# Optimization experiments

Measured on AMD Instinct MI355X. Metric: run time of the kernel, lower is better.

The kernel has to match this reference:

```python
import jax, jax.numpy as jnp
import numpy as np

Z = Y = X = 128
H = W = 256
FEAT_CH = 128
PE_DIM = 9
EMB = 128
B, V, NPTS = 2, 4, 65536


def make_grid_zyx():
    zs = jnp.linspace(-1.0, 1.0, Z)
    ys = jnp.linspace(-1.0, 1.0, Y)
    xs = jnp.linspace(-1.0, 1.0, X)
    gz, gy, gx = jnp.meshgrid(zs, ys, xs, indexing='ij')
    return jnp.stack([gz, gy, gx], axis=-1).reshape(-1, 3)  # (Z*Y*X, 3)


def fourier_pe(c):
    # coords + sin/cos at base frequency -> 3+3+3 = 9 dims
    return jnp.concatenate([c, jnp.sin(jnp.pi * c), jnp.cos(jnp.pi * c)], axis=-1)


def bilinear_sample(fm, py, px):
    # fm: (C,H,W); py,px: (n,) pixel coords (align_corners, border clamp) -> (n,C)
    px = jnp.clip(px, 0.0, W - 1.0)
    py = jnp.clip(py, 0.0, H - 1.0)
    x0 = jnp.clip(jnp.floor(px).astype(jnp.int32), 0, W - 2)
    y0 = jnp.clip(jnp.floor(py).astype(jnp.int32), 0, H - 2)
    x1, y1 = x0 + 1, y0 + 1
    wx = px - x0
    wy = py - y0
    f00 = fm[:, y0, x0]; f01 = fm[:, y0, x1]
    f10 = fm[:, y1, x0]; f11 = fm[:, y1, x1]
    top = f00 * (1.0 - wx) + f01 * wx
    bot = f10 * (1.0 - wx) + f11 * wx
    return (top * (1.0 - wy) + bot * wy).T


def inr_mlp(x, w_in, b_in, w1, b1, w2, b2, w_out, b_out):
    # pre-act residual MLP: num_blocks is small & static, loop is fine
    h = jax.nn.relu(x @ w_in + b_in)
    for i in range(w1.shape[0]):
        h = jax.nn.relu(h + jax.nn.relu(h @ w1[i] + b1[i]) @ w2[i] + b2[i])
    return h @ w_out + b_out


def setup_inputs() -> dict:
    key = jax.random.key(0)
    ks = jax.random.split(key, 24)
    s = 0.05
    n = lambda k, shp: jax.random.normal(k, shp, jnp.float32) * s
    return {
        'views': jax.random.normal(ks[0], (B, V, 1, H, W), jnp.float32),
        'angles': jax.random.uniform(ks[1], (B, V), jnp.float32, 0.0, 2.0 * np.pi),
        'idx': jax.random.randint(ks[2], (NPTS,), 0, Z * Y * X, jnp.int32),
        'conv_w': n(ks[3], (FEAT_CH, 1, 3, 3)),
        'conv_b': n(ks[4], (FEAT_CH,)),
        'vw_in': n(ks[5], (FEAT_CH + PE_DIM, 128)), 'vb_in': n(ks[6], (128,)),
        'vw1': n(ks[7], (3, 128, 128)), 'vb1': n(ks[8], (3, 128)),
        'vw2': n(ks[9], (3, 128, 128)), 'vb2': n(ks[10], (3, 128)),
        'vw_out': n(ks[11], (128, EMB)), 'vb_out': n(ks[12], (EMB,)),
        'gw_in': n(ks[13], (EMB, 128)), 'gb_in': n(ks[14], (128,)),
        'gw1': n(ks[15], (2, 128, 128)), 'gb1': n(ks[16], (2, 128)),
        'gw2': n(ks[17], (2, 128, 128)), 'gb2': n(ks[18], (2, 128)),
        'gw_out': n(ks[19], (128, 1)), 'gb_out': n(ks[20], (1,)),
    }


def reference(views, angles, idx, conv_w, conv_b, vw_in, vb_in, vw1, vb1, vw2, vb2,
              vw_out, vb_out, gw_in, gb_in, gw1, gb1, gw2, gb2, gw_out, gb_out):
    Bn, Vn = views.shape[0], views.shape[1]
    npts = idx.shape[0]
    # backbone (U-Net stand-in): 3x3 conv 1->feat_ch + ReLU
    x2d = views.reshape(Bn * Vn, 1, H, W)
    feats = jax.lax.conv_general_dilated(x2d, conv_w, (1, 1), 'SAME',
                                         dimension_numbers=('NCHW', 'OIHW', 'NCHW'))
    feats = jax.nn.relu(feats + conv_b[None, :, None, None]).reshape(Bn, Vn, FEAT_CH, H, W)
    # gather coords for requested voxels, positional encoding
    coords = make_grid_zyx()[idx]                      # (n,3) zyx in [-1,1]
    pe = fourier_pe(coords)                            # (n,9)
    z, y, x = coords[:, 0], coords[:, 1], coords[:, 2]
    ct = jnp.cos(angles)[..., None]                    # (B,V,1)
    st = jnp.sin(angles)[..., None]
    u = x[None, None, :] * ct - y[None, None, :] * st  # rotated in-plane coord (B,V,n)
    v = jnp.broadcast_to(z[None, None, :], u.shape)    # detector vertical = z
    px = (u + 1.0) * 0.5 * (W - 1)
    py = (v + 1.0) * 0.5 * (H - 1)
    f = jax.vmap(jax.vmap(bilinear_sample))(feats, py, px)        # (B,V,n,C)
    pe_b = jnp.broadcast_to(pe[None, None], (Bn, Vn, npts, PE_DIM))
    xin = jnp.concatenate([f, pe_b], axis=-1).reshape(Bn * Vn * npts, FEAT_CH + PE_DIM)
    r = inr_mlp(xin, vw_in, vb_in, vw1, vb1, vw2, vb2, vw_out, vb_out)
    r_mean = r.reshape(Bn, Vn, npts, EMB).mean(axis=1)            # sum over views / V
    yout = inr_mlp(r_mean.reshape(Bn * npts, EMB), gw_in, gb_in, gw1, gb1, gw2, gb2, gw_out, gb_out)
    return yout.reshape(Bn, npts)
```

## Files before the change

kernel.cpp:

```cpp
#include <hip/hip_runtime.h>
#include <math.h>

#define BB 2
#define VV 4
#define NPTSC 65536
#define HH 256
#define WW 256
#define CCH 128
#define PTS 32
#define ROWS (VV * PTS)

typedef __attribute__((ext_vector_type(8))) unsigned short ushort8;
typedef __attribute__((ext_vector_type(4))) unsigned short u16x4;
typedef __attribute__((ext_vector_type(8))) __bf16 bf16x8;
typedef __attribute__((ext_vector_type(4))) float floatx4;

__device__ unsigned short g_feats[(size_t)BB * VV * HH * WW * CCH];

__device__ __forceinline__ float b2f(unsigned short u) {
  unsigned int x = ((unsigned int)u) << 16;
  return __builtin_bit_cast(float, x);
}
__device__ __forceinline__ unsigned short f2b(float f) {
  return __builtin_bit_cast(unsigned short, (__bf16)f);
}

__global__ __launch_bounds__(256) void mvct_pc(
    const float* __restrict__ views, const float* __restrict__ conv_w,
    const float* __restrict__ conv_b,
    const float* __restrict__ vw_in, const float* __restrict__ vw1,
    const float* __restrict__ vw2, const float* __restrict__ vw_out,
    const float* __restrict__ gw_in, const float* __restrict__ gw1,
    const float* __restrict__ gw2, unsigned short* __restrict__ wbuf)
{
  if (blockIdx.x < 2048) {
    __shared__ float rows[2][3][132];
    const int h = threadIdx.x >> 7;
    const int c = threadIdx.x & 127;
    const int bv = blockIdx.x >> 8;
    const int y = blockIdx.x & 255;
    const int xb = h * 128;

    float w[9];
#pragma unroll
    for (int j = 0; j < 9; ++j) w[j] = conv_w[c * 9 + j];
    const float bias = conv_b[c];

    const float* img = views + (size_t)bv * HH * WW;
#pragma unroll
    for (int r = 0; r < 3; ++r) {
      int yy = y - 1 + r;
      for (int xcol = c; xcol < 130; xcol += 128) {
        int xx = xb - 1 + xcol;
        float v = 0.f;
        if (yy >= 0 && yy < HH && xx >= 0 && xx < WW) v = img[yy * WW + xx];
        rows[h][r][xcol] = v;
      }
    }
    __syncthreads();

    unsigned short* orow =
        g_feats + ((size_t)((bv * HH + y) * WW + xb)) * CCH + c;
    float a0 = rows[h][0][0], a1 = rows[h][1][0], a2 = rows[h][2][0];
    float b0 = rows[h][0][1], b1 = rows[h][1][1], b2 = rows[h][2][1];
#pragma unroll 8
    for (int x = 0; x < 128; ++x) {
      float c0 = rows[h][0][x + 2];
      float c1 = rows[h][1][x + 2];
      float c2 = rows[h][2][x + 2];
      float acc = bias
        + a0 * w[0] + b0 * w[1] + c0 * w[2]
        + a1 * w[3] + b1 * w[4] + c1 * w[5]
        + a2 * w[6] + b2 * w[7] + c2 * w[8];
      acc = fmaxf(acc, 0.f);
      orow[(size_t)x * CCH] = f2b(acc);
      a0 = b0; a1 = b1; a2 = b2;
      b0 = c0; b1 = c1; b2 = c2;
    }
  } else {
    int tid = (blockIdx.x - 2048) * 256 + threadIdx.x;
    if (tid >= 217088) return;
    float val;
    if (tid < 20480) {
      int n = tid / 160, k = tid - n * 160;
      val = (k < 137) ? vw_in[k * 128 + n] : 0.f;
    } else {
      int t = tid - 20480;
      const float* src;
      if (t < 49152) { src = vw1; }
      else if (t < 98304) { t -= 49152; src = vw2; }
      else if (t < 114688) { t -= 98304; src = vw_out; }
      else if (t < 131072) { t -= 114688; src = gw_in; }
      else if (t < 163840) { t -= 131072; src = gw1; }
      else { t -= 163840; src = gw2; }
      int i = t >> 14; int r = t & 16383; int n = r >> 7; int k = r & 127;
      val = src[i * 16384 + k * 128 + n];
    }
    wbuf[tid] = f2b(val);
  }
}

struct WReg {
  ushort8 a[2][4];
  floatx4 bs[2];
};

__device__ __forceinline__ WReg wload(const unsigned short* __restrict__ Wt,
                                      const float* __restrict__ bias,
                                      int lane, int ftBase) {
  WReg w;
  const int col = lane & 15, quad = lane >> 4;
#pragma unroll
  for (int ftl = 0; ftl < 2; ++ftl) {
    const int ft = ftBase + ftl;
#pragma unroll
    for (int kk = 0; kk < 4; ++kk)
      w.a[ftl][kk] = *(const ushort8*)(Wt + (ft * 16 + col) * 128 + kk * 32 + quad * 8);
    w.bs[ftl] = *(const floatx4*)(bias + ft * 16 + quad * 4);
  }
  return w;
}

template<int MODE, int NPT>
__device__ __forceinline__ void mlp_c(
    const unsigned short* Act, int lda, const WReg& w,
    const unsigned short* Res, int ldr,
    unsigned short* Dst, int ldd,
    float* racc, int lane, int ftBase)
{
  const int col = lane & 15, quad = lane >> 4;
  auto body = [&](int ptt) {
    ushort8 bfr[4];
#pragma unroll
    for (int kk = 0; kk < 4; ++kk)
      bfr[kk] = *(const ushort8*)(Act + (ptt * 16 + col) * lda + kk * 32 + quad * 8);
#pragma unroll
    for (int ftl = 0; ftl < 2; ++ftl) {
      const int ft = ftBase + ftl;
      floatx4 acc = {0.f, 0.f, 0.f, 0.f};
#pragma unroll
      for (int kk = 0; kk < 4; ++kk)
        acc = __builtin_amdgcn_mfma_f32_16x16x32_bf16(
            __builtin_bit_cast(bf16x8, w.a[ftl][kk]),
            __builtin_bit_cast(bf16x8, bfr[kk]), acc, 0, 0, 0);
      const int row = ptt * 16 + col;
      if constexpr (MODE == 2) {
#pragma unroll
        for (int r = 0; r < 4; ++r)
          racc[(ptt & 1) * 8 + ftl * 4 + r] += acc[r] + w.bs[ftl][r];
      } else {
        u16x4 rv;
        if constexpr (MODE == 1)
          rv = *(const u16x4*)(Res + row * ldr + ft * 16 + quad * 4);
        u16x4 o;
#pragma unroll
        for (int r = 0; r < 4; ++r) {
          float v = acc[r] + w.bs[ftl][r];
          if constexpr (MODE == 1) v += b2f(rv[r]);
          v = fmaxf(v, 0.f);
          o[r] = f2b(v);
        }
        *(u16x4*)(Dst + row * ldd + ft * 16 + quad * 4) = o;
      }
    }
  };
  if constexpr (MODE == 2) {
#pragma unroll
    for (int ptt = 0; ptt < NPT; ++ptt) body(ptt);
  } else {
#pragma unroll 2
    for (int ptt = 0; ptt < NPT; ++ptt) body(ptt);
  }
  __syncthreads();
}

__device__ __forceinline__ void mlp_first(
    const unsigned short* Act, int lda,
    const unsigned short* __restrict__ Wt, const float* __restrict__ bias,
    unsigned short* Dst, int ldd, int lane, int ftBase)
{
  const int col = lane & 15, quad = lane >> 4;
  ushort8 afr[2][5];
  floatx4 bs4[2];
#pragma unroll
  for (int ftl = 0; ftl < 2; ++ftl) {
    const int ft = ftBase + ftl;
#pragma unroll
    for (int kk = 0; kk < 5; ++kk)
      afr[ftl][kk] = *(const ushort8*)(Wt + (ft * 16 + col) * 160 + kk * 32 + quad * 8);
    bs4[ftl] = *(const floatx4*)(bias + ft * 16 + quad * 4);
  }
#pragma unroll 2
  for (int ptt = 0; ptt < (ROWS / 16); ++ptt) {
    ushort8 bfr[5];
#pragma unroll
    for (int kk = 0; kk < 5; ++kk)
      bfr[kk] = *(const ushort8*)(Act + (ptt * 16 + col) * lda + kk * 32 + quad * 8);
#pragma unroll
    for (int ftl = 0; ftl < 2; ++ftl) {
      const int ft = ftBase + ftl;
      floatx4 acc = {0.f, 0.f, 0.f, 0.f};
#pragma unroll
      for (int kk = 0; kk < 5; ++kk)
        acc = __builtin_amdgcn_mfma_f32_16x16x32_bf16(
            __builtin_bit_cast(bf16x8, afr[ftl][kk]),
            __builtin_bit_cast(bf16x8, bfr[kk]), acc, 0, 0, 0);
      const int row = ptt * 16 + col;
      u16x4 o;
#pragma unroll
      for (int r = 0; r < 4; ++r)
        o[r] = f2b(fmaxf(acc[r] + bs4[ftl][r], 0.f));
      *(u16x4*)(Dst + row * ldd + ft * 16 + quad * 4) = o;
    }
  }
  __syncthreads();
}

__global__ __launch_bounds__(256, 2) void mvct_main(
    const float* __restrict__ angles, const int* __restrict__ idx,
    const unsigned short* __restrict__ wbuf,
    const float* __restrict__ vb_in, const float* __restrict__ vb1,
    const float* __restrict__ vb2, const float* __restrict__ vb_out,
    const float* __restrict__ gb_in, const float* __restrict__ gb1,
    const float* __restrict__ gb2, const float* __restrict__ gw_out,
    const float* __restrict__ gb_out,
    float* __restrict__ out)
{
  __shared__ __align__(16) unsigned short X[ROWS][168];
  __shared__ __align__(16) unsigned short Hb[ROWS][136];
  const int tid = threadIdx.x;
  const int lane = tid & 63;
  const int ftBase = (tid >> 6) * 2;
  const int b = blockIdx.x >> 11;
  const int pts0 = (blockIdx.x & 2047) * PTS;

  const unsigned short* w_in_t   = wbuf;
  const unsigned short* vw1_t    = wbuf + 20480;
  const unsigned short* vw2_t    = wbuf + 69632;
  const unsigned short* vw_out_t = wbuf + 118784;
  const unsigned short* gw_in_t  = wbuf + 135168;
  const unsigned short* gw1_t    = wbuf + 151552;
  const unsigned short* gw2_t    = wbuf + 184320;

  const float inv = 2.0f / 127.0f;
  const int col = lane & 15, quad = lane >> 4;

  if (tid < ROWS) {
    int p = tid & (PTS - 1);
    int id = idx[pts0 + p];
    int iz = (id >> 14) & 127, iy = (id >> 7) & 127, ix = id & 127;
    float x = ix * inv - 1.f, y = iy * inv - 1.f, z = iz * inv - 1.f;
    const float PI = 3.14159265358979323846f;
    float pe[9] = {z, y, x, sinf(PI * z), sinf(PI * y), sinf(PI * x),
                   cosf(PI * z), cosf(PI * y), cosf(PI * x)};
#pragma unroll
    for (int j = 0; j < 9; ++j) X[tid][128 + j] = f2b(pe[j]);
    for (int j = 137; j < 160; ++j) X[tid][j] = 0;
  }

#pragma unroll
  for (int v = 0; v < VV; ++v) {
    const int bv = b * VV + v;
    const float ang = angles[bv];
    const float ct = cosf(ang), st = sinf(ang);
    const int cg = tid & 15;
#pragma unroll
    for (int ph = 0; ph < 2; ++ph) {
      const int p = ((tid >> 4) & 15) + ph * 16;
      int id = idx[pts0 + p];
      int iz = (id >> 14) & 127, iy = (id >> 7) & 127, ix = id & 127;
      float x = ix * inv - 1.f, y = iy * inv - 1.f, z = iz * inv - 1.f;
      float u = x * ct - y * st;
      float px = (u + 1.f) * 127.5f, py = (z + 1.f) * 127.5f;
      px = fminf(fmaxf(px, 0.f), 255.f);
      py = fminf(fmaxf(py, 0.f), 255.f);
      int x0 = min((int)px, 254), y0 = min((int)py, 254);
      float wx = px - (float)x0, wy = py - (float)y0;
      const unsigned short* bp =
          g_feats + ((size_t)((bv * HH + y0) * WW + x0)) * CCH + cg * 8;
      ushort8 q00 = *(const ushort8*)bp;
      ushort8 q01 = *(const ushort8*)(bp + CCH);
      ushort8 q10 = *(const ushort8*)(bp + WW * CCH);
      ushort8 q11 = *(const ushort8*)(bp + WW * CCH + CCH);
      float w00 = (1.f - wx) * (1.f - wy), w01 = wx * (1.f - wy);
      float w10 = (1.f - wx) * wy, w11 = wx * wy;
      ushort8 o;
#pragma unroll
      for (int j = 0; j < 8; ++j) {
        float f = w00 * b2f(q00[j]) + w01 * b2f(q01[j]) +
                  w10 * b2f(q10[j]) + w11 * b2f(q11[j]);
        o[j] = f2b(f);
      }
      *(ushort8*)&X[v * PTS + p][cg * 8] = o;
    }
  }
  __syncthreads();

  float racc[16];
#pragma unroll
  for (int i = 0; i < 16; ++i) racc[i] = 0.f;

  WReg wA = wload(vw1_t, vb1, lane, ftBase);
  mlp_first(&X[0][0], 168, w_in_t, vb_in, &Hb[0][0], 136, lane, ftBase);
  WReg wB = wload(vw2_t, vb2, lane, ftBase);
  mlp_c<0, 8>(&Hb[0][0], 136, wA, nullptr, 0, &X[0][0], 168, nullptr,
              lane, ftBase);
  wA = wload(vw1_t + 16384, vb1 + 128, lane, ftBase);
  mlp_c<1, 8>(&X[0][0], 168, wB, &Hb[0][0], 136, &Hb[0][0], 136, nullptr,
              lane, ftBase);
  wB = wload(vw2_t + 16384, vb2 + 128, lane, ftBase);
  mlp_c<0, 8>(&Hb[0][0], 136, wA, nullptr, 0, &X[0][0], 168, nullptr,
              lane, ftBase);
  wA = wload(vw1_t + 32768, vb1 + 256, lane, ftBase);
  mlp_c<1, 8>(&X[0][0], 168, wB, &Hb[0][0], 136, &Hb[0][0], 136, nullptr,
              lane, ftBase);
  wB = wload(vw2_t + 32768, vb2 + 256, lane, ftBase);
  mlp_c<0, 8>(&Hb[0][0], 136, wA, nullptr, 0, &X[0][0], 168, nullptr,
              lane, ftBase);
  wA = wload(vw_out_t, vb_out, lane, ftBase);
  mlp_c<1, 8>(&X[0][0], 168, wB, &Hb[0][0], 136, &Hb[0][0], 136, nullptr,
              lane, ftBase);
  wB = wload(gw_in_t, gb_in, lane, ftBase);
  mlp_c<2, 8>(&Hb[0][0], 136, wA, nullptr, 0, nullptr, 0, racc,
              lane, ftBase);

#pragma unroll
  for (int ph = 0; ph < 2; ++ph)
#pragma unroll
    for (int ftl = 0; ftl < 2; ++ftl) {
      u16x4 o;
#pragma unroll
      for (int r = 0; r < 4; ++r)
        o[r] = f2b(racc[ph * 8 + ftl * 4 + r] * 0.25f);
      *(u16x4*)(&X[ph * 16 + col][(ftBase + ftl) * 16 + quad * 4]) = o;
    }
  __syncthreads();

  wA = wload(gw1_t, gb1, lane, ftBase);
  mlp_c<0, 2>(&X[0][0], 168, wB, nullptr, 0, &Hb[0][0], 136, nullptr,
              lane, ftBase);
  wB = wload(gw2_t, gb2, lane, ftBase);
  mlp_c<0, 2>(&Hb[0][0], 136, wA, nullptr, 0, &X[0][0], 168, nullptr,
              lane, ftBase);
  wA = wload(gw1_t + 16384, gb1 + 128, lane, ftBase);
  mlp_c<1, 2>(&X[0][0], 168, wB, &Hb[0][0], 136, &Hb[0][0], 136, nullptr,
              lane, ftBase);
  wB = wload(gw2_t + 16384, gb2 + 128, lane, ftBase);
  mlp_c<0, 2>(&Hb[0][0], 136, wA, nullptr, 0, &X[0][0], 168, nullptr,
              lane, ftBase);
  mlp_c<1, 2>(&X[0][0], 168, wB, &Hb[0][0], 136, &Hb[0][0], 136, nullptr,
              lane, ftBase);

  if (tid < 128) {
    const int p = (tid & 15) + ((tid >> 6) << 4);
    const int q4 = (tid >> 4) & 3;
    float s = 0.f;
    const unsigned short* hr = &Hb[p][q4 * 32];
    const float* wo = gw_out + q4 * 32;
#pragma unroll
    for (int c = 0; c < 32; ++c)
      s += b2f(hr[c]) * wo[c];
    s += __shfl_xor(s, 16, 64);
    s += __shfl_xor(s, 32, 64);
    if (q4 == 0)
      out[(size_t)b * NPTSC + pts0 + p] = s + gb_out[0];
  }
}

extern "C" void kernel_launch(void* const* d_in, const int* in_sizes, int n_in,
                              void* d_out, int out_size, void* d_ws, size_t ws_size,
                              hipStream_t stream) {
  const float* views  = (const float*)d_in[0];
  const float* angles = (const float*)d_in[1];
  const int*   idx    = (const int*)d_in[2];
  const float* conv_w = (const float*)d_in[3];
  const float* conv_b = (const float*)d_in[4];
  const float* vw_in  = (const float*)d_in[5];
  const float* vb_in  = (const float*)d_in[6];
  const float* vw1    = (const float*)d_in[7];
  const float* vb1    = (const float*)d_in[8];
  const float* vw2    = (const float*)d_in[9];
  const float* vb2    = (const float*)d_in[10];
  const float* vw_out = (const float*)d_in[11];
  const float* vb_out = (const float*)d_in[12];
  const float* gw_in  = (const float*)d_in[13];
  const float* gb_in  = (const float*)d_in[14];
  const float* gw1    = (const float*)d_in[15];
  const float* gb1    = (const float*)d_in[16];
  const float* gw2    = (const float*)d_in[17];
  const float* gb2    = (const float*)d_in[18];
  const float* gw_out = (const float*)d_in[19];
  const float* gb_out = (const float*)d_in[20];

  unsigned short* wbuf = (unsigned short*)d_ws;

  hipLaunchKernelGGL(mvct_pc, dim3(2896), dim3(256), 0, stream,
                     views, conv_w, conv_b,
                     vw_in, vw1, vw2, vw_out, gw_in, gw1, gw2, wbuf);
  hipLaunchKernelGGL(mvct_main, dim3(BB * (NPTSC / PTS)), dim3(256), 0, stream,
                     angles, idx, wbuf, vb_in, vb1, vb2, vb_out,
                     gb_in, gb1, gb2, gw_out, gb_out,
                     (float*)d_out);
}
```

Measured before the change: 395.0 us.

## Double main-kernel block to 512 threads, splitting MLP rows across two wave groups

The main kernel now launches 512 threads per block. Waves are split into two row halves, each handling 64 of the 128 view rows (and 16 of the 32 points in the global MLP), so each wave does half the MFMA work per layer. Weights are loaded inside each layer instead of being prefetched one layer ahead, and the bias is folded into the MFMA accumulator's initial value. The view-mean reduction now combines partial sums from the two halves through a float scratch area in shared memory, with an extra barrier. The trade is more waves per block and higher launch-bounds occupancy against losing the weight prefetch overlap and adding sync and scratch traffic.

```diff
diff --git a/kernel.cpp b/kernel.cpp
--- a/kernel.cpp
+++ b/kernel.cpp
@@ -123,31 +123,33 @@
 
 template<int MODE, int NPT>
 __device__ __forceinline__ void mlp_c(
-    const unsigned short* Act, int lda, const WReg& w,
+    const unsigned short* Act, int lda,
+    const unsigned short* __restrict__ Wt, const float* __restrict__ bias,
     const unsigned short* Res, int ldr,
     unsigned short* Dst, int ldd,
-    float* racc, int lane, int ftBase)
+    float* racc, int lane, int ftBase, int rowBase)
 {
   const int col = lane & 15, quad = lane >> 4;
+  WReg w = wload(Wt, bias, lane, ftBase);
   auto body = [&](int ptt) {
+    const int row = rowBase + ptt * 16 + col;
     ushort8 bfr[4];
 #pragma unroll
     for (int kk = 0; kk < 4; ++kk)
-      bfr[kk] = *(const ushort8*)(Act + (ptt * 16 + col) * lda + kk * 32 + quad * 8);
+      bfr[kk] = *(const ushort8*)(Act + row * lda + kk * 32 + quad * 8);
 #pragma unroll
     for (int ftl = 0; ftl < 2; ++ftl) {
       const int ft = ftBase + ftl;
-      floatx4 acc = {0.f, 0.f, 0.f, 0.f};
+      floatx4 acc = w.bs[ftl];
 #pragma unroll
       for (int kk = 0; kk < 4; ++kk)
         acc = __builtin_amdgcn_mfma_f32_16x16x32_bf16(
             __builtin_bit_cast(bf16x8, w.a[ftl][kk]),
             __builtin_bit_cast(bf16x8, bfr[kk]), acc, 0, 0, 0);
-      const int row = ptt * 16 + col;
       if constexpr (MODE == 2) {
 #pragma unroll
         for (int r = 0; r < 4; ++r)
-          racc[(ptt & 1) * 8 + ftl * 4 + r] += acc[r] + w.bs[ftl][r];
+          racc[(ptt & 1) * 8 + ftl * 4 + r] += acc[r];
       } else {
         u16x4 rv;
         if constexpr (MODE == 1)
@@ -155,7 +157,7 @@
         u16x4 o;
 #pragma unroll
         for (int r = 0; r < 4; ++r) {
-          float v = acc[r] + w.bs[ftl][r];
+          float v = acc[r];
           if constexpr (MODE == 1) v += b2f(rv[r]);
           v = fmaxf(v, 0.f);
           o[r] = f2b(v);
@@ -177,7 +179,7 @@
 __device__ __forceinline__ void mlp_first(
     const unsigned short* Act, int lda,
     const unsigned short* __restrict__ Wt, const float* __restrict__ bias,
-    unsigned short* Dst, int ldd, int lane, int ftBase)
+    unsigned short* Dst, int ldd, int lane, int ftBase, int rowBase)
 {
   const int col = lane & 15, quad = lane >> 4;
   ushort8 afr[2][5];
@@ -191,32 +193,32 @@
     bs4[ftl] = *(const floatx4*)(bias + ft * 16 + quad * 4);
   }
 #pragma unroll 2
-  for (int ptt = 0; ptt < (ROWS / 16); ++ptt) {
+  for (int ptt = 0; ptt < 4; ++ptt) {
+    const int row = rowBase + ptt * 16 + col;
     ushort8 bfr[5];
 #pragma unroll
     for (int kk = 0; kk < 5; ++kk)
-      bfr[kk] = *(const ushort8*)(Act + (ptt * 16 + col) * lda + kk * 32 + quad * 8);
+      bfr[kk] = *(const ushort8*)(Act + row * lda + kk * 32 + quad * 8);
 #pragma unroll
     for (int ftl = 0; ftl < 2; ++ftl) {
       const int ft = ftBase + ftl;
-      floatx4 acc = {0.f, 0.f, 0.f, 0.f};
+      floatx4 acc = bs4[ftl];
 #pragma unroll
       for (int kk = 0; kk < 5; ++kk)
         acc = __builtin_amdgcn_mfma_f32_16x16x32_bf16(
             __builtin_bit_cast(bf16x8, afr[ftl][kk]),
             __builtin_bit_cast(bf16x8, bfr[kk]), acc, 0, 0, 0);
-      const int row = ptt * 16 + col;
       u16x4 o;
 #pragma unroll
       for (int r = 0; r < 4; ++r)
-        o[r] = f2b(fmaxf(acc[r] + bs4[ftl][r], 0.f));
+        o[r] = f2b(fmaxf(acc[r], 0.f));
       *(u16x4*)(Dst + row * ldd + ft * 16 + quad * 4) = o;
     }
   }
   __syncthreads();
 }
 
-__global__ __launch_bounds__(256, 2) void mvct_main(
+__global__ __launch_bounds__(512, 4) void mvct_main(
     const float* __restrict__ angles, const int* __restrict__ idx,
     const unsigned short* __restrict__ wbuf,
     const float* __restrict__ vb_in, const float* __restrict__ vb1,
@@ -230,7 +232,10 @@
   __shared__ __align__(16) unsigned short Hb[ROWS][136];
   const int tid = threadIdx.x;
   const int lane = tid & 63;
-  const int ftBase = (tid >> 6) * 2;
+  const int wav = tid >> 6;
+  const int rh = wav >> 2;
+  const int ftBase = (wav & 3) * 2;
+  const int rowBase = rh * 64;
   const int b = blockIdx.x >> 11;
   const int pts0 = (blockIdx.x & 2047) * PTS;
 
@@ -258,18 +263,17 @@
     for (int j = 137; j < 160; ++j) X[tid][j] = 0;
   }
 
-#pragma unroll
-  for (int v = 0; v < VV; ++v) {
-    const int bv = b * VV + v;
-    const float ang = angles[bv];
-    const float ct = cosf(ang), st = sinf(ang);
+  {
     const int cg = tid & 15;
-#pragma unroll
-    for (int ph = 0; ph < 2; ++ph) {
-      const int p = ((tid >> 4) & 15) + ph * 16;
-      int id = idx[pts0 + p];
-      int iz = (id >> 14) & 127, iy = (id >> 7) & 127, ix = id & 127;
-      float x = ix * inv - 1.f, y = iy * inv - 1.f, z = iz * inv - 1.f;
+    const int p = (tid >> 4) & 31;
+    const int id = idx[pts0 + p];
+    const int iz = (id >> 14) & 127, iy = (id >> 7) & 127, ix = id & 127;
+    const float x = ix * inv - 1.f, y = iy * inv - 1.f, z = iz * inv - 1.f;
+#pragma unroll
+    for (int v = 0; v < VV; ++v) {
+      const int bv = b * VV + v;
+      const float ang = angles[bv];
+      const float ct = cosf(ang), st = sinf(ang);
       float u = x * ct - y * st;
       float px = (u + 1.f) * 127.5f, py = (z + 1.f) * 127.5f;
       px = fminf(fmaxf(px, 0.f), 255.f);
@@ -300,56 +304,62 @@
 #pragma unroll
   for (int i = 0; i < 16; ++i) racc[i] = 0.f;
 
-  WReg wA = wload(vw1_t, vb1, lane, ftBase);
-  mlp_first(&X[0][0], 168, w_in_t, vb_in, &Hb[0][0], 136, lane, ftBase);
-  WReg wB = wload(vw2_t, vb2, lane, ftBase);
-  mlp_c<0, 8>(&Hb[0][0], 136, wA, nullptr, 0, &X[0][0], 168, nullptr,
-              lane, ftBase);
-  wA = wload(vw1_t + 16384, vb1 + 128, lane, ftBase);
-  mlp_c<1, 8>(&X[0][0], 168, wB, &Hb[0][0], 136, &Hb[0][0], 136, nullptr,
-              lane, ftBase);
-  wB = wload(vw2_t + 16384, vb2 + 128, lane, ftBase);
-  mlp_c<0, 8>(&Hb[0][0], 136, wA, nullptr, 0, &X[0][0], 168, nullptr,
-              lane, ftBase);
-  wA = wload(vw1_t + 32768, vb1 + 256, lane, ftBase);
-  mlp_c<1, 8>(&X[0][0], 168, wB, &Hb[0][0], 136, &Hb[0][0], 136, nullptr,
-              lane, ftBase);
-  wB = wload(vw2_t + 32768, vb2 + 256, lane, ftBase);
-  mlp_c<0, 8>(&Hb[0][0], 136, wA, nullptr, 0, &X[0][0], 168, nullptr,
-              lane, ftBase);
-  wA = wload(vw_out_t, vb_out, lane, ftBase);
-  mlp_c<1, 8>(&X[0][0], 168, wB, &Hb[0][0], 136, &Hb[0][0], 136, nullptr,
-              lane, ftBase);
-  wB = wload(gw_in_t, gb_in, lane, ftBase);
-  mlp_c<2, 8>(&Hb[0][0], 136, wA, nullptr, 0, nullptr, 0, racc,
-              lane, ftBase);
-
-#pragma unroll
-  for (int ph = 0; ph < 2; ++ph)
-#pragma unroll
-    for (int ftl = 0; ftl < 2; ++ftl) {
-      u16x4 o;
-#pragma unroll
-      for (int r = 0; r < 4; ++r)
-        o[r] = f2b(racc[ph * 8 + ftl * 4 + r] * 0.25f);
-      *(u16x4*)(&X[ph * 16 + col][(ftBase + ftl) * 16 + quad * 4]) = o;
-    }
+  mlp_first(&X[0][0], 168, w_in_t, vb_in, &Hb[0][0], 136, lane, ftBase, rowBase);
+  mlp_c<0, 4>(&Hb[0][0], 136, vw1_t, vb1, nullptr, 0, &X[0][0], 168,
+              nullptr, lane, ftBase, rowBase);
+  mlp_c<1, 4>(&X[0][0], 168, vw2_t, vb2, &Hb[0][0], 136, &Hb[0][0], 136,
+              nullptr, lane, ftBase, rowBase);
+  mlp_c<0, 4>(&Hb[0][0], 136, vw1_t + 16384, vb1 + 128, nullptr, 0, &X[0][0], 168,
+              nullptr, lane, ftBase, rowBase);
+  mlp_c<1, 4>(&X[0][0], 168, vw2_t + 16384, vb2 + 128, &Hb[0][0], 136, &Hb[0][0], 136,
+              nullptr, lane, ftBase, rowBase);
+  mlp_c<0, 4>(&Hb[0][0], 136, vw1_t + 32768, vb1 + 256, nullptr, 0, &X[0][0], 168,
+              nullptr, lane, ftBase, rowBase);
+  mlp_c<1, 4>(&X[0][0], 168, vw2_t + 32768, vb2 + 256, &Hb[0][0], 136, &Hb[0][0], 136,
+              nullptr, lane, ftBase, rowBase);
+  mlp_c<2, 4>(&Hb[0][0], 136, vw_out_t, vb_out, nullptr, 0, nullptr, 0,
+              racc, lane, ftBase, rowBase);
+
+  float* scr = (float*)((char*)&X[0][0] + 32 * 168 * 2);
+  if (rh == 1) {
+#pragma unroll
+    for (int ph = 0; ph < 2; ++ph)
+#pragma unroll
+      for (int ftl = 0; ftl < 2; ++ftl) {
+        floatx4 v4;
+#pragma unroll
+        for (int r = 0; r < 4; ++r) v4[r] = racc[ph * 8 + ftl * 4 + r];
+        *(floatx4*)&scr[(ph * 16 + col) * 132 + (ftBase + ftl) * 16 + quad * 4] = v4;
+      }
+  }
   __syncthreads();
-
-  wA = wload(gw1_t, gb1, lane, ftBase);
-  mlp_c<0, 2>(&X[0][0], 168, wB, nullptr, 0, &Hb[0][0], 136, nullptr,
-              lane, ftBase);
-  wB = wload(gw2_t, gb2, lane, ftBase);
-  mlp_c<0, 2>(&Hb[0][0], 136, wA, nullptr, 0, &X[0][0], 168, nullptr,
-              lane, ftBase);
-  wA = wload(gw1_t + 16384, gb1 + 128, lane, ftBase);
-  mlp_c<1, 2>(&X[0][0], 168, wB, &Hb[0][0], 136, &Hb[0][0], 136, nullptr,
-              lane, ftBase);
-  wB = wload(gw2_t + 16384, gb2 + 128, lane, ftBase);
-  mlp_c<0, 2>(&Hb[0][0], 136, wA, nullptr, 0, &X[0][0], 168, nullptr,
-              lane, ftBase);
-  mlp_c<1, 2>(&X[0][0], 168, wB, &Hb[0][0], 136, &Hb[0][0], 136, nullptr,
-              lane, ftBase);
+  if (rh == 0) {
+#pragma unroll
+    for (int ph = 0; ph < 2; ++ph)
+#pragma unroll
+      for (int ftl = 0; ftl < 2; ++ftl) {
+        floatx4 pv = *(const floatx4*)&scr[(ph * 16 + col) * 132 +
+                                           (ftBase + ftl) * 16 + quad * 4];
+        u16x4 o;
+#pragma unroll
+        for (int r = 0; r < 4; ++r)
+          o[r] = f2b((racc[ph * 8 + ftl * 4 + r] + pv[r]) * 0.25f);
+        *(u16x4*)(&X[ph * 16 + col][(ftBase + ftl) * 16 + quad * 4]) = o;
+      }
+  }
+  __syncthreads();
+
+  const int gBase = rh * 16;
+  mlp_c<0, 1>(&X[0][0], 168, gw_in_t, gb_in, nullptr, 0, &Hb[0][0], 136,
+              nullptr, lane, ftBase, gBase);
+  mlp_c<0, 1>(&Hb[0][0], 136, gw1_t, gb1, nullptr, 0, &X[0][0], 168,
+              nullptr, lane, ftBase, gBase);
+  mlp_c<1, 1>(&X[0][0], 168, gw2_t, gb2, &Hb[0][0], 136, &Hb[0][0], 136,
+              nullptr, lane, ftBase, gBase);
+  mlp_c<0, 1>(&Hb[0][0], 136, gw1_t + 16384, gb1 + 128, nullptr, 0, &X[0][0], 168,
+              nullptr, lane, ftBase, gBase);
+  mlp_c<1, 1>(&X[0][0], 168, gw2_t + 16384, gb2 + 128, &Hb[0][0], 136, &Hb[0][0], 136,
+              nullptr, lane, ftBase, gBase);
 
   if (tid < 128) {
     const int p = (tid & 15) + ((tid >> 6) << 4);
@@ -397,7 +407,7 @@
   hipLaunchKernelGGL(mvct_pc, dim3(2896), dim3(256), 0, stream,
                      views, conv_w, conv_b,
                      vw_in, vw1, vw2, vw_out, gw_in, gw1, gw2, wbuf);
-  hipLaunchKernelGGL(mvct_main, dim3(BB * (NPTSC / PTS)), dim3(256), 0, stream,
+  hipLaunchKernelGGL(mvct_main, dim3(BB * (NPTSC / PTS)), dim3(512), 0, stream,
                      angles, idx, wbuf, vb_in, vb1, vb2, vb_out,
                      gb_in, gb1, gb2, gw_out, gb_out,
                      (float*)d_out);
```

Result: slower. 563.8 us (+42.7%).

## Halve points per block and give each wave four feature tiles

Applied to the files above, without the earlier changes.

Each block now handles 16 points with 128 threads (two waves) instead of 32 points with 256 threads. Each wave now owns four 16-wide output-feature tiles rather than two, so it holds twice as many weight fragments in registers. The bias is also folded into the MFMA accumulator's initial value, which removes the separate per-element bias add. The intent is a smaller per-block footprint and more blocks for scheduling. In exchange, weights are reloaded from memory for every 16 points, and register pressure per wave roughly doubles.

```diff
diff --git a/kernel.cpp b/kernel.cpp
--- a/kernel.cpp
+++ b/kernel.cpp
@@ -7,7 +7,7 @@
 #define HH 256
 #define WW 256
 #define CCH 128
-#define PTS 32
+#define PTS 16
 #define ROWS (VV * PTS)
 
 typedef __attribute__((ext_vector_type(8))) unsigned short ushort8;
@@ -100,18 +100,18 @@
   }
 }
 
-struct WReg {
-  ushort8 a[2][4];
-  floatx4 bs[2];
+struct WReg4 {
+  ushort8 a[4][4];
+  floatx4 bs[4];
 };
 
-__device__ __forceinline__ WReg wload(const unsigned short* __restrict__ Wt,
-                                      const float* __restrict__ bias,
-                                      int lane, int ftBase) {
-  WReg w;
+__device__ __forceinline__ WReg4 wload4(const unsigned short* __restrict__ Wt,
+                                        const float* __restrict__ bias,
+                                        int lane, int ftBase) {
+  WReg4 w;
   const int col = lane & 15, quad = lane >> 4;
 #pragma unroll
-  for (int ftl = 0; ftl < 2; ++ftl) {
+  for (int ftl = 0; ftl < 4; ++ftl) {
     const int ft = ftBase + ftl;
 #pragma unroll
     for (int kk = 0; kk < 4; ++kk)
@@ -123,31 +123,31 @@
 
 template<int MODE, int NPT>
 __device__ __forceinline__ void mlp_c(
-    const unsigned short* Act, int lda, const WReg& w,
+    const unsigned short* Act, int lda, const WReg4& w,
     const unsigned short* Res, int ldr,
     unsigned short* Dst, int ldd,
     float* racc, int lane, int ftBase)
 {
   const int col = lane & 15, quad = lane >> 4;
   auto body = [&](int ptt) {
+    const int row = ptt * 16 + col;
     ushort8 bfr[4];
 #pragma unroll
     for (int kk = 0; kk < 4; ++kk)
-      bfr[kk] = *(const ushort8*)(Act + (ptt * 16 + col) * lda + kk * 32 + quad * 8);
-#pragma unroll
-    for (int ftl = 0; ftl < 2; ++ftl) {
+      bfr[kk] = *(const ushort8*)(Act + row * lda + kk * 32 + quad * 8);
+#pragma unroll
+    for (int ftl = 0; ftl < 4; ++ftl) {
       const int ft = ftBase + ftl;
-      floatx4 acc = {0.f, 0.f, 0.f, 0.f};
+      floatx4 acc = w.bs[ftl];
 #pragma unroll
       for (int kk = 0; kk < 4; ++kk)
         acc = __builtin_amdgcn_mfma_f32_16x16x32_bf16(
             __builtin_bit_cast(bf16x8, w.a[ftl][kk]),
             __builtin_bit_cast(bf16x8, bfr[kk]), acc, 0, 0, 0);
-      const int row = ptt * 16 + col;
       if constexpr (MODE == 2) {
 #pragma unroll
         for (int r = 0; r < 4; ++r)
-          racc[(ptt & 1) * 8 + ftl * 4 + r] += acc[r] + w.bs[ftl][r];
+          racc[ftl * 4 + r] += acc[r];
       } else {
         u16x4 rv;
         if constexpr (MODE == 1)
@@ -155,7 +155,7 @@
         u16x4 o;
 #pragma unroll
         for (int r = 0; r < 4; ++r) {
-          float v = acc[r] + w.bs[ftl][r];
+          float v = acc[r];
           if constexpr (MODE == 1) v += b2f(rv[r]);
           v = fmaxf(v, 0.f);
           o[r] = f2b(v);
@@ -180,10 +180,10 @@
     unsigned short* Dst, int ldd, int lane, int ftBase)
 {
   const int col = lane & 15, quad = lane >> 4;
-  ushort8 afr[2][5];
-  floatx4 bs4[2];
-#pragma unroll
-  for (int ftl = 0; ftl < 2; ++ftl) {
+  ushort8 afr[4][5];
+  floatx4 bs4[4];
+#pragma unroll
+  for (int ftl = 0; ftl < 4; ++ftl) {
     const int ft = ftBase + ftl;
 #pragma unroll
     for (int kk = 0; kk < 5; ++kk)
@@ -192,31 +192,31 @@
   }
 #pragma unroll 2
   for (int ptt = 0; ptt < (ROWS / 16); ++ptt) {
+    const int row = ptt * 16 + col;
     ushort8 bfr[5];
 #pragma unroll
     for (int kk = 0; kk < 5; ++kk)
-      bfr[kk] = *(const ushort8*)(Act + (ptt * 16 + col) * lda + kk * 32 + quad * 8);
-#pragma unroll
-    for (int ftl = 0; ftl < 2; ++ftl) {
+      bfr[kk] = *(const ushort8*)(Act + row * lda + kk * 32 + quad * 8);
+#pragma unroll
+    for (int ftl = 0; ftl < 4; ++ftl) {
       const int ft = ftBase + ftl;
-      floatx4 acc = {0.f, 0.f, 0.f, 0.f};
+      floatx4 acc = bs4[ftl];
 #pragma unroll
       for (int kk = 0; kk < 5; ++kk)
         acc = __builtin_amdgcn_mfma_f32_16x16x32_bf16(
             __builtin_bit_cast(bf16x8, afr[ftl][kk]),
             __builtin_bit_cast(bf16x8, bfr[kk]), acc, 0, 0, 0);
-      const int row = ptt * 16 + col;
       u16x4 o;
 #pragma unroll
       for (int r = 0; r < 4; ++r)
-        o[r] = f2b(fmaxf(acc[r] + bs4[ftl][r], 0.f));
+        o[r] = f2b(fmaxf(acc[r], 0.f));
       *(u16x4*)(Dst + row * ldd + ft * 16 + quad * 4) = o;
     }
   }
   __syncthreads();
 }
 
-__global__ __launch_bounds__(256, 2) void mvct_main(
+__global__ __launch_bounds__(128, 2) void mvct_main(
     const float* __restrict__ angles, const int* __restrict__ idx,
     const unsigned short* __restrict__ wbuf,
     const float* __restrict__ vb_in, const float* __restrict__ vb1,
@@ -230,9 +230,9 @@
   __shared__ __align__(16) unsigned short Hb[ROWS][136];
   const int tid = threadIdx.x;
   const int lane = tid & 63;
-  const int ftBase = (tid >> 6) * 2;
-  const int b = blockIdx.x >> 11;
-  const int pts0 = (blockIdx.x & 2047) * PTS;
+  const int ftBase = (tid >> 6) * 4;
+  const int b = blockIdx.x >> 12;
+  const int pts0 = (blockIdx.x & 4095) * PTS;
 
   const unsigned short* w_in_t   = wbuf;
   const unsigned short* vw1_t    = wbuf + 20480;
@@ -266,7 +266,7 @@
     const int cg = tid & 15;
 #pragma unroll
     for (int ph = 0; ph < 2; ++ph) {
-      const int p = ((tid >> 4) & 15) + ph * 16;
+      const int p = ((tid >> 4) & 7) + ph * 8;
       int id = idx[pts0 + p];
       int iz = (id >> 14) & 127, iy = (id >> 7) & 127, ix = id & 127;
       float x = ix * inv - 1.f, y = iy * inv - 1.f, z = iz * inv - 1.f;
@@ -300,60 +300,57 @@
 #pragma unroll
   for (int i = 0; i < 16; ++i) racc[i] = 0.f;
 
-  WReg wA = wload(vw1_t, vb1, lane, ftBase);
+  WReg4 wA = wload4(vw1_t, vb1, lane, ftBase);
   mlp_first(&X[0][0], 168, w_in_t, vb_in, &Hb[0][0], 136, lane, ftBase);
-  WReg wB = wload(vw2_t, vb2, lane, ftBase);
-  mlp_c<0, 8>(&Hb[0][0], 136, wA, nullptr, 0, &X[0][0], 168, nullptr,
-              lane, ftBase);
-  wA = wload(vw1_t + 16384, vb1 + 128, lane, ftBase);
-  mlp_c<1, 8>(&X[0][0], 168, wB, &Hb[0][0], 136, &Hb[0][0], 136, nullptr,
-              lane, ftBase);
-  wB = wload(vw2_t + 16384, vb2 + 128, lane, ftBase);
-  mlp_c<0, 8>(&Hb[0][0], 136, wA, nullptr, 0, &X[0][0], 168, nullptr,
-              lane, ftBase);
-  wA = wload(vw1_t + 32768, vb1 + 256, lane, ftBase);
-  mlp_c<1, 8>(&X[0][0], 168, wB, &Hb[0][0], 136, &Hb[0][0], 136, nullptr,
-              lane, ftBase);
-  wB = wload(vw2_t + 32768, vb2 + 256, lane, ftBase);
-  mlp_c<0, 8>(&Hb[0][0], 136, wA, nullptr, 0, &X[0][0], 168, nullptr,
-              lane, ftBase);
-  wA = wload(vw_out_t, vb_out, lane, ftBase);
-  mlp_c<1, 8>(&X[0][0], 168, wB, &Hb[0][0], 136, &Hb[0][0], 136, nullptr,
-              lane, ftBase);
-  wB = wload(gw_in_t, gb_in, lane, ftBase);
-  mlp_c<2, 8>(&Hb[0][0], 136, wA, nullptr, 0, nullptr, 0, racc,
-              lane, ftBase);
-
-#pragma unroll
-  for (int ph = 0; ph < 2; ++ph)
-#pragma unroll
-    for (int ftl = 0; ftl < 2; ++ftl) {
-      u16x4 o;
-#pragma unroll
-      for (int r = 0; r < 4; ++r)
-        o[r] = f2b(racc[ph * 8 + ftl * 4 + r] * 0.25f);
-      *(u16x4*)(&X[ph * 16 + col][(ftBase + ftl) * 16 + quad * 4]) = o;
-    }
+  WReg4 wB = wload4(vw2_t, vb2, lane, ftBase);
+  mlp_c<0, 4>(&Hb[0][0], 136, wA, nullptr, 0, &X[0][0], 168, nullptr,
+              lane, ftBase);
+  wA = wload4(vw1_t + 16384, vb1 + 128, lane, ftBase);
+  mlp_c<1, 4>(&X[0][0], 168, wB, &Hb[0][0], 136, &Hb[0][0], 136, nullptr,
+              lane, ftBase);
+  wB = wload4(vw2_t + 16384, vb2 + 128, lane, ftBase);
+  mlp_c<0, 4>(&Hb[0][0], 136, wA, nullptr, 0, &X[0][0], 168, nullptr,
+              lane, ftBase);
+  wA = wload4(vw1_t + 32768, vb1 + 256, lane, ftBase);
+  mlp_c<1, 4>(&X[0][0], 168, wB, &Hb[0][0], 136, &Hb[0][0], 136, nullptr,
+              lane, ftBase);
+  wB = wload4(vw2_t + 32768, vb2 + 256, lane, ftBase);
+  mlp_c<0, 4>(&Hb[0][0], 136, wA, nullptr, 0, &X[0][0], 168, nullptr,
+              lane, ftBase);
+  wA = wload4(vw_out_t, vb_out, lane, ftBase);
+  mlp_c<1, 4>(&X[0][0], 168, wB, &Hb[0][0], 136, &Hb[0][0], 136, nullptr,
+              lane, ftBase);
+  wB = wload4(gw_in_t, gb_in, lane, ftBase);
+  mlp_c<2, 4>(&Hb[0][0], 136, wA, nullptr, 0, nullptr, 0, racc,
+              lane, ftBase);
+
+  wA = wload4(gw1_t, gb1, lane, ftBase);
+#pragma unroll
+  for (int ftl = 0; ftl < 4; ++ftl) {
+    u16x4 o;
+#pragma unroll
+    for (int r = 0; r < 4; ++r)
+      o[r] = f2b(racc[ftl * 4 + r] * 0.25f);
+    *(u16x4*)(&X[col][(ftBase + ftl) * 16 + quad * 4]) = o;
+  }
   __syncthreads();
 
-  wA = wload(gw1_t, gb1, lane, ftBase);
-  mlp_c<0, 2>(&X[0][0], 168, wB, nullptr, 0, &Hb[0][0], 136, nullptr,
-              lane, ftBase);
-  wB = wload(gw2_t, gb2, lane, ftBase);
-  mlp_c<0, 2>(&Hb[0][0], 136, wA, nullptr, 0, &X[0][0], 168, nullptr,
-              lane, ftBase);
-  wA = wload(gw1_t + 16384, gb1 + 128, lane, ftBase);
-  mlp_c<1, 2>(&X[0][0], 168, wB, &Hb[0][0], 136, &Hb[0][0], 136, nullptr,
-              lane, ftBase);
-  wB = wload(gw2_t + 16384, gb2 + 128, lane, ftBase);
-  mlp_c<0, 2>(&Hb[0][0], 136, wA, nullptr, 0, &X[0][0], 168, nullptr,
-              lane, ftBase);
-  mlp_c<1, 2>(&X[0][0], 168, wB, &Hb[0][0], 136, &Hb[0][0], 136, nullptr,
-              lane, ftBase);
-
-  if (tid < 128) {
-    const int p = (tid & 15) + ((tid >> 6) << 4);
-    const int q4 = (tid >> 4) & 3;
+  mlp_c<0, 1>(&X[0][0], 168, wB, nullptr, 0, &Hb[0][0], 136, nullptr,
+              lane, ftBase);
+  wB = wload4(gw2_t, gb2, lane, ftBase);
+  mlp_c<0, 1>(&Hb[0][0], 136, wA, nullptr, 0, &X[0][0], 168, nullptr,
+              lane, ftBase);
+  wA = wload4(gw1_t + 16384, gb1 + 128, lane, ftBase);
+  mlp_c<1, 1>(&X[0][0], 168, wB, &Hb[0][0], 136, &Hb[0][0], 136, nullptr,
+              lane, ftBase);
+  wB = wload4(gw2_t + 16384, gb2 + 128, lane, ftBase);
+  mlp_c<0, 1>(&Hb[0][0], 136, wA, nullptr, 0, &X[0][0], 168, nullptr,
+              lane, ftBase);
+  mlp_c<1, 1>(&X[0][0], 168, wB, &Hb[0][0], 136, &Hb[0][0], 136, nullptr,
+              lane, ftBase);
+
+  if (tid < 64) {
+    const int p = tid & 15, q4 = tid >> 4;
     float s = 0.f;
     const unsigned short* hr = &Hb[p][q4 * 32];
     const float* wo = gw_out + q4 * 32;
@@ -397,7 +394,7 @@
   hipLaunchKernelGGL(mvct_pc, dim3(2896), dim3(256), 0, stream,
                      views, conv_w, conv_b,
                      vw_in, vw1, vw2, vw_out, gw_in, gw1, gw2, wbuf);
-  hipLaunchKernelGGL(mvct_main, dim3(BB * (NPTSC / PTS)), dim3(256), 0, stream,
+  hipLaunchKernelGGL(mvct_main, dim3(BB * (NPTSC / PTS)), dim3(128), 0, stream,
                      angles, idx, wbuf, vb_in, vb1, vb2, vb_out,
                      gb_in, gb1, gb2, gw_out, gb_out,
                      (float*)d_out);
```

After: 545.7 us. 38.2% more time.
